# Optimization experiments

Hardware: AMD Instinct MI355X
Metric: run time of the kernel (lower is better)

Reference implementation:

```python
import jax, jax.numpy as jnp
import numpy as np

EPS = 1e-5
NH_MHA = 8
NH_GCN = 4


def _ln(x, w, b):
    m = x.mean(-1, keepdims=True)
    v = ((x - m) ** 2).mean(-1, keepdims=True)
    return (x - m) * jax.lax.rsqrt(v + EPS) * w + b


def _mha(t, in_w, in_b, out_w, out_b):
    # torch nn.MultiheadAttention (batch_first, eval mode -> no dropout)
    B, N, C = t.shape
    hd = C // NH_MHA
    qkv = t @ in_w.T + in_b
    q, k, v = jnp.split(qkv, 3, axis=-1)
    q = q.reshape(B, N, NH_MHA, hd)
    k = k.reshape(B, N, NH_MHA, hd)
    v = v.reshape(B, N, NH_MHA, hd)
    s = jnp.einsum('bihd,bjhd->bhij', q, k) * (1.0 / np.sqrt(hd))
    a = jax.nn.softmax(s, axis=-1)
    o = jnp.einsum('bhij,bjhd->bihd', a, v).reshape(B, N, C)
    return o @ out_w.T + out_b


def _gcn(x, v_w, v_b, e1_w, e1_b, eln_w, eln_b, e2_w, e2_b, o_w, o_b, n_w, n_b):
    # GraphConvolutionNetwork.forward (query/key branches are computed but
    # unused in the original -> omitted, identical math)
    B, N, C = x.shape
    hd = C // NH_GCN
    # edge MLP: split first linear so the [B,N,N,2C] concat is never built
    w1a, w1b = e1_w[:, :C], e1_w[:, C:]
    e = (x @ w1a.T)[:, :, None, :] + (x @ w1b.T)[:, None, :, :] + e1_b  # [B,N,N,C]
    e = jax.nn.gelu(_ln(e, eln_w, eln_b), approximate=False)
    ew = e @ e2_w.T + e2_b                 # [B,Ni,Nj,H]
    adj = jax.nn.softmax(ew, axis=2)       # softmax over Nj (== dim=-1 after permute in torch)
    v = (x @ v_w.T + v_b).reshape(B, N, NH_GCN, hd)
    out = jnp.einsum('bijh,bjhd->bihd', adj, v).reshape(B, N, C)
    out = out @ o_w.T + o_b
    return _ln(out + x, n_w, n_b)          # in_features == out_features -> residual


def reference(x, mha_in_w, mha_in_b, mha_out_w, mha_out_b,
              g0_v_w, g0_v_b, g0_e1_w, g0_e1_b, g0_eln_w, g0_eln_b, g0_e2_w, g0_e2_b, g0_o_w, g0_o_b, g0_n_w, g0_n_b,
              g1_v_w, g1_v_b, g1_e1_w, g1_e1_b, g1_eln_w, g1_eln_b, g1_e2_w, g1_e2_b, g1_o_w, g1_o_b, g1_n_w, g1_n_b,
              n1_w, n1_b, n2_w, n2_b,
              f1_w, f1_b, fln_w, fln_b, f2_w, f2_b):
    B, C, H, W = x.shape
    tokens = x.reshape(B, C, H * W).transpose(0, 2, 1)  # b c h w -> b (h w) c
    attn = _mha(tokens, mha_in_w, mha_in_b, mha_out_w, mha_out_b)
    attn = _ln(attn + tokens, n1_w, n1_b)
    g = _gcn(attn, g0_v_w, g0_v_b, g0_e1_w, g0_e1_b, g0_eln_w, g0_eln_b, g0_e2_w, g0_e2_b, g0_o_w, g0_o_b, g0_n_w, g0_n_b)
    g = _gcn(g, g1_v_w, g1_v_b, g1_e1_w, g1_e1_b, g1_eln_w, g1_eln_b, g1_e2_w, g1_e2_b, g1_o_w, g1_o_b, g1_n_w, g1_n_b)
    g = _ln(g, n2_w, n2_b)
    cat = jnp.concatenate([attn, g], axis=-1)           # [B,N,2C]
    f = cat @ f1_w.T + f1_b
    f = jax.nn.gelu(_ln(f, fln_w, fln_b), approximate=False)
    f = f @ f2_w.T + f2_b
    out = tokens + f
    return out.transpose(0, 2, 1).reshape(B, C, H, W)


def setup_inputs() -> dict:
    key = jax.random.key(0)
    ks = jax.random.split(key, 8)
    B, C, H, W = 2, 128, 24, 24
    f32 = jnp.float32

    def w(k, shape):
        return jax.random.normal(k, shape, f32) * 0.02

    d = {"x": jax.random.normal(ks[0], (B, C, H, W), f32)}
    d["mha_in_w"] = w(ks[1], (3 * C, C)); d["mha_in_b"] = jnp.zeros((3 * C,), f32)
    d["mha_out_w"] = w(ks[2], (C, C)); d["mha_out_b"] = jnp.zeros((C,), f32)
    for i in range(2):
        kk = jax.random.split(ks[3 + i], 4)
        p = f"g{i}_"
        d[p + "v_w"] = w(kk[0], (C, C)); d[p + "v_b"] = jnp.zeros((C,), f32)
        d[p + "e1_w"] = w(kk[1], (C, 2 * C)); d[p + "e1_b"] = jnp.zeros((C,), f32)
        d[p + "eln_w"] = jnp.ones((C,), f32); d[p + "eln_b"] = jnp.zeros((C,), f32)
        d[p + "e2_w"] = w(kk[2], (NH_GCN, C)); d[p + "e2_b"] = jnp.zeros((NH_GCN,), f32)
        d[p + "o_w"] = w(kk[3], (C, C)); d[p + "o_b"] = jnp.zeros((C,), f32)
        d[p + "n_w"] = jnp.ones((C,), f32); d[p + "n_b"] = jnp.zeros((C,), f32)
    d["n1_w"] = jnp.ones((C,), f32); d["n1_b"] = jnp.zeros((C,), f32)
    d["n2_w"] = jnp.ones((C,), f32); d["n2_b"] = jnp.zeros((C,), f32)
    d["f1_w"] = w(ks[5], (C, 2 * C)); d["f1_b"] = jnp.zeros((C,), f32)
    d["fln_w"] = jnp.ones((C,), f32); d["fln_b"] = jnp.zeros((C,), f32)
    d["f2_w"] = w(ks[6], (C, C)); d["f2_b"] = jnp.zeros((C,), f32)
    return d
```

## Files before the change

### kernel.cpp

```cpp
#include <hip/hip_runtime.h>
#include <hip/hip_fp16.h>
#include <math.h>

#define NN 576
#define EPSV 1e-5f

typedef _Float16 h2v __attribute__((ext_vector_type(2)));
__device__ __forceinline__ float fdot2f(__half2 a, __half2 b, float c) {
    return __builtin_amdgcn_fdot2(__builtin_bit_cast(h2v, a),
                                  __builtin_bit_cast(h2v, b), c, false);
}

__device__ __forceinline__ float gelu_exact(float x) {
    return 0.5f * x * (1.0f + erff(x * 0.70710678118654752f));
}

__global__ void k_tok(const float* __restrict__ x, float* __restrict__ tok) {
    int b = blockIdx.y;
    int idx = blockIdx.x * 256 + threadIdx.x;
    if (idx < NN * 128) {
        int n = idx >> 7, c = idx & 127;
        tok[(size_t)b * NN * 128 + idx] = x[((size_t)b * 128 + c) * NN + n];
    }
}

__global__ void k_prep(const float* __restrict__ mha_in_w,
                       const float* __restrict__ e1w0, const float* __restrict__ vw0,
                       const float* __restrict__ e1w1, const float* __restrict__ vw1,
                       const float* __restrict__ lnw0, const float* __restrict__ lnb0,
                       const float* __restrict__ e2w0,
                       const float* __restrict__ lnw1, const float* __restrict__ lnb1,
                       const float* __restrict__ e2w1,
                       float* __restrict__ wTq, float* __restrict__ wT0,
                       float* __restrict__ wT1, __half* __restrict__ wh) {
    int which = blockIdx.y;
    int idx = blockIdx.x * 256 + threadIdx.x;
    if (which == 3) {
        if (idx < 1536) {
            int l = idx / 768, i2 = idx - l * 768;
            const float* lw = l ? lnw1 : lnw0;
            const float* lb = l ? lnb1 : lnb0;
            const float* e2 = l ? e2w1 : e2w0;
            float v;
            if (i2 < 128)      v = lw[i2];
            else if (i2 < 256) v = lb[i2 - 128];
            else               v = e2[i2 - 256];
            wh[idx] = __float2half(v);
        }
        return;
    }
    int k = idx / 384, o = idx - k * 384;
    if (which == 0) {
        wTq[idx] = mha_in_w[o * 128 + k];
    } else {
        const float* e1w = (which == 1) ? e1w0 : e1w1;
        const float* vw  = (which == 1) ? vw0  : vw1;
        float v;
        if (o < 128)      v = e1w[o * 256 + k];
        else if (o < 256) v = e1w[(o - 128) * 256 + 128 + k];
        else              v = vw[(o - 256) * 128 + k];
        ((which == 1) ? wT0 : wT1)[idx] = v;
    }
}

template<bool CENTER>
__global__ __launch_bounds__(384) void k_gemmT(
    const float* __restrict__ A, const float* __restrict__ wT,
    const float* __restrict__ b0, const float* __restrict__ b1, const float* __restrict__ b2,
    float* __restrict__ out)
{
    const int t = threadIdx.x;
    const int r0 = blockIdx.x * 4;
    __shared__ float a_s[4][132];
    if (t < 128) {
        float4 v = *(const float4*)(A + (size_t)(r0 + (t >> 5)) * 128 + (t & 31) * 4);
        *(float4*)&a_s[t >> 5][(t & 31) * 4] = v;
    }
    __syncthreads();
    float acc[4] = {0.f, 0.f, 0.f, 0.f};
    #pragma unroll 8
    for (int k = 0; k < 128; ++k) {
        float w = wT[(size_t)k * 384 + t];
        acc[0] += a_s[0][k] * w;
        acc[1] += a_s[1][k] * w;
        acc[2] += a_s[2][k] * w;
        acc[3] += a_s[3][k] * w;
    }
    const float* bp = (t < 128) ? b0 : ((t < 256) ? b1 : b2);
    float bv = bp ? bp[t & 127] : 0.f;
    #pragma unroll
    for (int r = 0; r < 4; ++r) acc[r] += bv;

    if (CENTER) {
        __shared__ float redc[6][4];
        const int wv = t >> 6, ln = t & 63;
        #pragma unroll
        for (int r = 0; r < 4; ++r) {
            float xr = acc[r];
            #pragma unroll
            for (int off = 32; off > 0; off >>= 1) xr += __shfl_xor(xr, off);
            if (ln == 0) redc[wv][r] = xr;
        }
        __syncthreads();
        if (t < 256) {
            const int ch = t >> 7;
            #pragma unroll
            for (int r = 0; r < 4; ++r) {
                float mean = (redc[2 * ch][r] + redc[2 * ch + 1][r]) * (1.0f / 128.0f);
                acc[r] -= mean;
            }
        }
    }
    if (t < 256) {
        #pragma unroll
        for (int r = 0; r < 4; ++r)
            ((__half*)(out + (size_t)(r0 + r) * 384))[t] = __float2half(acc[r]);
    } else {
        #pragma unroll
        for (int r = 0; r < 4; ++r)
            out[(size_t)(r0 + r) * 384 + t] = acc[r];
    }
}

__global__ __launch_bounds__(256) void k_score(
    const float* __restrict__ qkv, __half* __restrict__ sc)
{
    const int jt = blockIdx.x, it = blockIdx.y, b = blockIdx.z;
    const int i0 = it * 16, j0 = jt * 16;
    const int t = threadIdx.x;
    __shared__ __half q_s[16][136], k_s[16][136];
    for (int idx = t; idx < 512; idx += 256) {
        int tile = idx >> 8, r = (idx >> 4) & 15, cq = idx & 15;
        const __half* src = (const __half*)(qkv + (size_t)(b * NN + (tile ? j0 : i0) + r) * 384)
                            + (tile ? 128 : 0) + cq * 8;
        __half* dst = tile ? &k_s[r][cq * 8] : &q_s[r][cq * 8];
        *(uint4*)dst = *(const uint4*)src;
    }
    __syncthreads();
    const int ti = t >> 4, tj = t & 15;
    const uint4* qr = (const uint4*)q_s[ti];
    const uint4* kr = (const uint4*)k_s[tj];
    float acc[8] = {0.f,0.f,0.f,0.f,0.f,0.f,0.f,0.f};
    #pragma unroll
    for (int sstep = 0; sstep < 16; ++sstep) {
        uint4 q4 = qr[sstep], k4 = kr[sstep];
        const __half2* qh = (const __half2*)&q4;
        const __half2* kh = (const __half2*)&k4;
        #pragma unroll
        for (int p = 0; p < 4; ++p)
            acc[sstep >> 1] = fdot2f(qh[p], kh[p], acc[sstep >> 1]);
    }
    __half2 h[4];
    #pragma unroll
    for (int p = 0; p < 4; ++p)
        h[p] = __floats2half2_rn(acc[2 * p] * 0.25f, acc[2 * p + 1] * 0.25f);
    *(uint4*)(sc + ((size_t)(b * NN + i0 + ti) * NN + j0 + tj) * 8) = *(uint4*)h;
}

__global__ __launch_bounds__(256) void k_edge(
    const float* __restrict__ qkv, const __half* __restrict__ wh,
    const float* __restrict__ e2b, __half* __restrict__ ew)
{
    const int jt = blockIdx.x, it = blockIdx.y, b = blockIdx.z;
    const int i0 = it * 16, j0 = jt * 16;
    const int t = threadIdx.x;
    __shared__ __half ua_s[16][136], wb_s[16][136], wh_s[768];

    for (int idx = t; idx < 512; idx += 256) {
        int tile = idx >> 8, r = (idx >> 4) & 15, cq = idx & 15;
        const __half* src = (const __half*)(qkv + (size_t)(b * NN + (tile ? j0 : i0) + r) * 384)
                            + (tile ? 128 : 0) + cq * 8;
        __half* dst = tile ? &wb_s[r][cq * 8] : &ua_s[r][cq * 8];
        *(uint4*)dst = *(const uint4*)src;
    }
    if (t < 96) *(uint4*)&wh_s[t * 8] = *(const uint4*)&wh[t * 8];
    __syncthreads();

    const int ti = t >> 4, tj = t & 15;
    const uint4* uar = (const uint4*)ua_s[ti];
    const uint4* wbr = (const uint4*)wb_s[tj];

    float s2 = 0.f;
    #pragma unroll
    for (int sstep = 0; sstep < 16; ++sstep) {
        uint4 u4 = uar[sstep], w4 = wbr[sstep];
        const __half2* uh = (const __half2*)&u4;
        const __half2* whp = (const __half2*)&w4;
        #pragma unroll
        for (int p = 0; p < 4; ++p) {
            __half2 e = __hadd2(uh[p], whp[p]);
            s2 = fdot2f(e, e, s2);
        }
    }
    const float rstd = rsqrtf(s2 * (1.0f / 128.0f) + EPSV);
    const __half2 rh   = __float2half2_rn(rstd);
    const __half2 cexp = __float2half2_rn(-2.4554672f);
    const __half2 one2 = __float2half2_rn(1.0f);

    float p0 = 0.f, p1 = 0.f, p2 = 0.f, p3 = 0.f;
    #pragma unroll 4
    for (int sstep = 0; sstep < 16; ++sstep) {
        uint4 u4 = uar[sstep], w4 = wbr[sstep];
        uint4 lw4 = *(const uint4*)&wh_s[sstep * 8];
        uint4 lb4 = *(const uint4*)&wh_s[128 + sstep * 8];
        uint4 q04 = *(const uint4*)&wh_s[256 + sstep * 8];
        uint4 q14 = *(const uint4*)&wh_s[384 + sstep * 8];
        uint4 q24 = *(const uint4*)&wh_s[512 + sstep * 8];
        uint4 q34 = *(const uint4*)&wh_s[640 + sstep * 8];
        const __half2* uh  = (const __half2*)&u4;
        const __half2* whp = (const __half2*)&w4;
        const __half2* lwh = (const __half2*)&lw4;
        const __half2* lbh = (const __half2*)&lb4;
        const __half2* q0h = (const __half2*)&q04;
        const __half2* q1h = (const __half2*)&q14;
        const __half2* q2h = (const __half2*)&q24;
        const __half2* q3h = (const __half2*)&q34;
        #pragma unroll
        for (int p = 0; p < 4; ++p) {
            __half2 e   = __hadd2(uh[p], whp[p]);
            __half2 rlw = __hmul2(rh, lwh[p]);
            __half2 nrm = __hfma2(e, rlw, lbh[p]);
            __half2 z   = __hmul2(nrm, cexp);
            __half2 ex  = h2exp2(z);
            __half2 den = __hadd2(ex, one2);
            __half2 rr  = h2rcp(den);
            __half2 g   = __hmul2(nrm, rr);
            p0 = fdot2f(g, q0h[p], p0);
            p1 = fdot2f(g, q1h[p], p1);
            p2 = fdot2f(g, q2h[p], p2);
            p3 = fdot2f(g, q3h[p], p3);
        }
    }
    __half2 h01 = __floats2half2_rn(p0 + e2b[0], p1 + e2b[1]);
    __half2 h23 = __floats2half2_rn(p2 + e2b[2], p3 + e2b[3]);
    __half* dst = ew + ((size_t)(b * NN + i0 + ti) * NN + j0 + tj) * 4;
    *(__half2*)dst = h01;
    *(__half2*)(dst + 2) = h23;
}

template<int NH>
__global__ __launch_bounds__(256) void k_agg(
    const float* __restrict__ resid, const float* __restrict__ vbuf,
    const __half* __restrict__ sc,
    const float* __restrict__ ow, const float* __restrict__ ob,
    const float* __restrict__ nw, const float* __restrict__ nb,
    float* __restrict__ outp)
{
    constexpr int GL = 256 / NH;
    constexpr int NE = NN / GL;
    const int bi = blockIdx.x;
    const int b = bi / NN, i = bi - b * NN;
    const int t = threadIdx.x;

    __shared__ float st_m[NH], st_i[NH];
    __shared__ float aggp[8][128];
    __shared__ float agg_s[128];
    __shared__ float op[2][128];
    __shared__ float red1[4], red2[4];

    const __half* srow = sc + (size_t)(b * NN + i) * NN * NH;

    {
        const int h = t / GL, jl = t % GL;
        float sv[NE];
        #pragma unroll
        for (int k = 0; k < NE; ++k)
            sv[k] = __half2float(srow[(size_t)(jl + k * GL) * NH + h]);
        float mx = -1e30f;
        #pragma unroll
        for (int k = 0; k < NE; ++k) mx = fmaxf(mx, sv[k]);
        #pragma unroll
        for (int off = GL / 2; off > 0; off >>= 1) mx = fmaxf(mx, __shfl_xor(mx, off));
        float sm = 0.f;
        #pragma unroll
        for (int k = 0; k < NE; ++k) sm += __expf(sv[k] - mx);
        #pragma unroll
        for (int off = GL / 2; off > 0; off >>= 1) sm += __shfl_xor(sm, off);
        if (jl == 0) { st_m[h] = mx; st_i[h] = 1.0f / sm; }
    }
    __syncthreads();

    {
        const int c4 = (t & 31) * 4, jg = t >> 5;
        const int h2 = c4 >> ((NH == 8) ? 4 : 5);
        const float m2 = st_m[h2], inv2 = st_i[h2];
        float4 acc = {0.f, 0.f, 0.f, 0.f};
        const float* vb = vbuf + 256 + c4;
        #pragma unroll 4
        for (int j = jg; j < NN; j += 8) {
            float p = __expf(__half2float(srow[(size_t)j * NH + h2]) - m2);
            const float4 v4 = *(const float4*)(vb + (size_t)(b * NN + j) * 384);
            acc.x += p * v4.x; acc.y += p * v4.y; acc.z += p * v4.z; acc.w += p * v4.w;
        }
        acc.x *= inv2; acc.y *= inv2; acc.z *= inv2; acc.w *= inv2;
        *(float4*)&aggp[jg][c4] = acc;
    }
    __syncthreads();
    if (t < 128) {
        float s = 0.f;
        #pragma unroll
        for (int gq = 0; gq < 8; ++gq) s += aggp[gq][t];
        agg_s[t] = s;
    }
    __syncthreads();

    {
        const int c = t & 127, half = t >> 7;
        float o = 0.f;
        const float4* wr = (const float4*)(ow + (size_t)c * 128 + half * 64);
        const float4* ar = (const float4*)(agg_s + half * 64);
        #pragma unroll
        for (int kq = 0; kq < 16; ++kq) {
            float4 w = wr[kq], a = ar[kq];
            o += w.x * a.x + w.y * a.y + w.z * a.z + w.w * a.w;
        }
        op[half][c] = o;
    }
    __syncthreads();
    float val = 0.f;
    if (t < 128)
        val = op[0][t] + op[1][t] + ob[t] + resid[(size_t)(b * NN + i) * 128 + t];

    float s1 = val, s2 = val * val;
    #pragma unroll
    for (int off = 32; off > 0; off >>= 1) {
        s1 += __shfl_xor(s1, off);
        s2 += __shfl_xor(s2, off);
    }
    if ((t & 63) == 0) { red1[t >> 6] = s1; red2[t >> 6] = s2; }
    __syncthreads();
    float tot1 = red1[0] + red1[1] + red1[2] + red1[3];
    float tot2 = red2[0] + red2[1] + red2[2] + red2[3];
    float mean = tot1 * (1.0f / 128.0f);
    float var = tot2 * (1.0f / 128.0f) - mean * mean;
    float rstd = rsqrtf(var + EPSV);
    if (t < 128)
        outp[(size_t)(b * NN + i) * 128 + t] = (val - mean) * rstd * nw[t] + nb[t];
}

__global__ __launch_bounds__(128) void k_final(
    const float* __restrict__ tok, const float* __restrict__ attn, const float* __restrict__ g,
    const float* __restrict__ n2w, const float* __restrict__ n2b,
    const float* __restrict__ f1w, const float* __restrict__ f1b,
    const float* __restrict__ flnw, const float* __restrict__ flnb,
    const float* __restrict__ f2w, const float* __restrict__ f2b,
    float* __restrict__ out)
{
    const int bi = blockIdx.x;
    const int b = bi / NN, i = bi - b * NN;
    const int t = threadIdx.x;
    __shared__ float cat_s[256];
    __shared__ float gl_s[128];
    __shared__ float red1[2], red2[2];

    const size_t row = (size_t)(b * NN + i) * 128;
    cat_s[t] = attn[row + t];
    float gv = g[row + t];
    {
        float s1 = gv, s2 = gv * gv;
        #pragma unroll
        for (int off = 32; off > 0; off >>= 1) { s1 += __shfl_xor(s1, off); s2 += __shfl_xor(s2, off); }
        if ((t & 63) == 0) { red1[t >> 6] = s1; red2[t >> 6] = s2; }
        __syncthreads();
        float mean = (red1[0] + red1[1]) * (1.0f / 128.0f);
        float var = (red2[0] + red2[1]) * (1.0f / 128.0f) - mean * mean;
        float rstd = rsqrtf(var + EPSV);
        cat_s[128 + t] = (gv - mean) * rstd * n2w[t] + n2b[t];
    }
    __syncthreads();
    float f = f1b[t];
    {
        const float4* wr = reinterpret_cast<const float4*>(f1w + (size_t)t * 256);
        const float4* cr = reinterpret_cast<const float4*>(cat_s);
        #pragma unroll 8
        for (int kq = 0; kq < 64; ++kq) {
            float4 w = wr[kq], c = cr[kq];
            f += w.x * c.x + w.y * c.y + w.z * c.z + w.w * c.w;
        }
    }
    {
        float s1 = f, s2 = f * f;
        #pragma unroll
        for (int off = 32; off > 0; off >>= 1) { s1 += __shfl_xor(s1, off); s2 += __shfl_xor(s2, off); }
        __syncthreads();
        if ((t & 63) == 0) { red1[t >> 6] = s1; red2[t >> 6] = s2; }
        __syncthreads();
        float mean = (red1[0] + red1[1]) * (1.0f / 128.0f);
        float var = (red2[0] + red2[1]) * (1.0f / 128.0f) - mean * mean;
        float rstd = rsqrtf(var + EPSV);
        float nrm = (f - mean) * rstd * flnw[t] + flnb[t];
        gl_s[t] = gelu_exact(nrm);
    }
    __syncthreads();
    float o = f2b[t];
    {
        const float4* wr = reinterpret_cast<const float4*>(f2w + (size_t)t * 128);
        const float4* gr = reinterpret_cast<const float4*>(gl_s);
        #pragma unroll 8
        for (int kq = 0; kq < 32; ++kq) {
            float4 w = wr[kq], gg = gr[kq];
            o += w.x * gg.x + w.y * gg.y + w.z * gg.z + w.w * gg.w;
        }
    }
    out[((size_t)b * 128 + t) * NN + i] = tok[row + t] + o;
}

extern "C" void kernel_launch(void* const* d_in, const int* in_sizes, int n_in,
                              void* d_out, int out_size, void* d_ws, size_t ws_size,
                              hipStream_t stream) {
    const float* x         = (const float*)d_in[0];
    const float* mha_in_b  = (const float*)d_in[2];
    const float* mha_out_w = (const float*)d_in[3];
    const float* mha_out_b = (const float*)d_in[4];
    const float* gv_w[2]  = {(const float*)d_in[5],  (const float*)d_in[17]};
    const float* gv_b[2]  = {(const float*)d_in[6],  (const float*)d_in[18]};
    const float* ge1_w[2] = {(const float*)d_in[7],  (const float*)d_in[19]};
    const float* ge1_b[2] = {(const float*)d_in[8],  (const float*)d_in[20]};
    const float* geln_w[2]= {(const float*)d_in[9],  (const float*)d_in[21]};
    const float* geln_b[2]= {(const float*)d_in[10], (const float*)d_in[22]};
    const float* ge2_w[2] = {(const float*)d_in[11], (const float*)d_in[23]};
    const float* ge2_b[2] = {(const float*)d_in[12], (const float*)d_in[24]};
    const float* go_w[2]  = {(const float*)d_in[13], (const float*)d_in[25]};
    const float* go_b[2]  = {(const float*)d_in[14], (const float*)d_in[26]};
    const float* gn_w[2]  = {(const float*)d_in[15], (const float*)d_in[27]};
    const float* gn_b[2]  = {(const float*)d_in[16], (const float*)d_in[28]};
    const float* n1w = (const float*)d_in[29];
    const float* n1b = (const float*)d_in[30];
    const float* n2w = (const float*)d_in[31];
    const float* n2b = (const float*)d_in[32];
    const float* f1w = (const float*)d_in[33];
    const float* f1b = (const float*)d_in[34];
    const float* flnw = (const float*)d_in[35];
    const float* flnb = (const float*)d_in[36];
    const float* f2w = (const float*)d_in[37];
    const float* f2b = (const float*)d_in[38];

    float* ws     = (float*)d_ws;
    float* tokens = ws;
    float* attn   = tokens + 147456;
    float* g      = attn + 147456;
    float* qkv    = g + 147456;
    float* wTq    = qkv + 442368;
    float* wT0    = wTq + 49152;
    float* wT1    = wT0 + 49152;
    __half* wh    = (__half*)(wT1 + 49152);
    __half* sc    = wh + 2048;
    __half* ewh   = sc;

    k_tok<<<dim3(288, 2), 256, 0, stream>>>(x, tokens);
    k_prep<<<dim3(192, 4), 256, 0, stream>>>((const float*)d_in[1],
        ge1_w[0], gv_w[0], ge1_w[1], gv_w[1],
        geln_w[0], geln_b[0], ge2_w[0],
        geln_w[1], geln_b[1], ge2_w[1],
        wTq, wT0, wT1, wh);

    k_gemmT<false><<<288, 384, 0, stream>>>(tokens, wTq,
        mha_in_b, mha_in_b + 128, mha_in_b + 256, qkv);
    k_score<<<dim3(36, 36, 2), 256, 0, stream>>>(qkv, sc);
    k_agg<8><<<1152, 256, 0, stream>>>(tokens, qkv, sc, mha_out_w, mha_out_b,
                                       n1w, n1b, attn);

    for (int l = 0; l < 2; ++l) {
        const float* xin = (l == 0) ? attn : g;
        const float* wTl = (l == 0) ? wT0 : wT1;
        k_gemmT<true><<<288, 384, 0, stream>>>(xin, wTl,
            nullptr, ge1_b[l], gv_b[l], qkv);
        k_edge<<<dim3(36, 36, 2), 256, 0, stream>>>(qkv, wh + l * 768,
                                                    ge2_b[l], ewh);
        k_agg<4><<<1152, 256, 0, stream>>>(xin, qkv, ewh, go_w[l], go_b[l],
                                           gn_w[l], gn_b[l], g);
    }
    k_final<<<1152, 128, 0, stream>>>(tokens, attn, g, n2w, n2b,
        f1w, f1b, flnw, flnb, f2w, f2b, (float*)d_out);
}
```

Baseline: 229.2 us.

## Fuse setup kernels, fold final FFN into last aggregation, cache softmax probs in LDS

Merges the token transpose and weight prep into one setup launch, and fuses the final norm/FFN stage into the last GCN aggregation kernel so the final layer output never goes through global memory. The aggregation kernel now keeps exponentiated scores as fp16 in shared memory instead of re-reading scores and recomputing exp in the value pass. The edge kernel reorders the LayerNorm multiply. The changes cut launches and redundant exp/global reads, at the cost of more shared memory per block (lower occupancy) and fp16 rounding of the probabilities.

```diff
diff --git a/kernel.cpp b/kernel.cpp
--- a/kernel.cpp
+++ b/kernel.cpp
@@ -4,6 +4,7 @@
 
 #define NN 576
 #define EPSV 1e-5f
+#define PSTR 592
 
 typedef _Float16 h2v __attribute__((ext_vector_type(2)));
 __device__ __forceinline__ float fdot2f(__half2 a, __half2 b, float c) {
@@ -15,27 +16,26 @@
     return 0.5f * x * (1.0f + erff(x * 0.70710678118654752f));
 }
 
-__global__ void k_tok(const float* __restrict__ x, float* __restrict__ tok) {
-    int b = blockIdx.y;
-    int idx = blockIdx.x * 256 + threadIdx.x;
-    if (idx < NN * 128) {
-        int n = idx >> 7, c = idx & 127;
-        tok[(size_t)b * NN * 128 + idx] = x[((size_t)b * 128 + c) * NN + n];
-    }
-}
-
-__global__ void k_prep(const float* __restrict__ mha_in_w,
-                       const float* __restrict__ e1w0, const float* __restrict__ vw0,
-                       const float* __restrict__ e1w1, const float* __restrict__ vw1,
-                       const float* __restrict__ lnw0, const float* __restrict__ lnb0,
-                       const float* __restrict__ e2w0,
-                       const float* __restrict__ lnw1, const float* __restrict__ lnb1,
-                       const float* __restrict__ e2w1,
-                       float* __restrict__ wTq, float* __restrict__ wT0,
-                       float* __restrict__ wT1, __half* __restrict__ wh) {
-    int which = blockIdx.y;
-    int idx = blockIdx.x * 256 + threadIdx.x;
-    if (which == 3) {
+__global__ void k_setup(const float* __restrict__ x, float* __restrict__ tok,
+                        const float* __restrict__ mha_in_w,
+                        const float* __restrict__ e1w0, const float* __restrict__ vw0,
+                        const float* __restrict__ e1w1, const float* __restrict__ vw1,
+                        const float* __restrict__ lnw0, const float* __restrict__ lnb0,
+                        const float* __restrict__ e2w0,
+                        const float* __restrict__ lnw1, const float* __restrict__ lnb1,
+                        const float* __restrict__ e2w1,
+                        float* __restrict__ wTq, float* __restrict__ wT0,
+                        float* __restrict__ wT1, __half* __restrict__ wh) {
+    const int which = blockIdx.y;
+    const int idx = blockIdx.x * 256 + threadIdx.x;
+    if (which < 2) {
+        if (idx < NN * 128) {
+            int n = idx >> 7, c = idx & 127;
+            tok[(size_t)which * NN * 128 + idx] = x[((size_t)which * 128 + c) * NN + n];
+        }
+        return;
+    }
+    if (which == 5) {
         if (idx < 1536) {
             int l = idx / 768, i2 = idx - l * 768;
             const float* lw = l ? lnw1 : lnw0;
@@ -49,17 +49,18 @@
         }
         return;
     }
+    if (idx >= 49152) return;
     int k = idx / 384, o = idx - k * 384;
-    if (which == 0) {
+    if (which == 2) {
         wTq[idx] = mha_in_w[o * 128 + k];
     } else {
-        const float* e1w = (which == 1) ? e1w0 : e1w1;
-        const float* vw  = (which == 1) ? vw0  : vw1;
+        const float* e1w = (which == 3) ? e1w0 : e1w1;
+        const float* vw  = (which == 3) ? vw0  : vw1;
         float v;
         if (o < 128)      v = e1w[o * 256 + k];
         else if (o < 256) v = e1w[(o - 128) * 256 + 128 + k];
         else              v = vw[(o - 256) * 128 + k];
-        ((which == 1) ? wT0 : wT1)[idx] = v;
+        ((which == 3) ? wT0 : wT1)[idx] = v;
     }
 }
 
@@ -218,8 +219,8 @@
         #pragma unroll
         for (int p = 0; p < 4; ++p) {
             __half2 e   = __hadd2(uh[p], whp[p]);
-            __half2 rlw = __hmul2(rh, lwh[p]);
-            __half2 nrm = __hfma2(e, rlw, lbh[p]);
+            __half2 t1  = __hmul2(e, lwh[p]);
+            __half2 nrm = __hfma2(t1, rh, lbh[p]);
             __half2 z   = __hmul2(nrm, cexp);
             __half2 ex  = h2exp2(z);
             __half2 den = __hadd2(ex, one2);
@@ -238,13 +239,19 @@
     *(__half2*)(dst + 2) = h23;
 }
 
-template<int NH>
+template<int NH, bool FINAL>
 __global__ __launch_bounds__(256) void k_agg(
     const float* __restrict__ resid, const float* __restrict__ vbuf,
     const __half* __restrict__ sc,
     const float* __restrict__ ow, const float* __restrict__ ob,
     const float* __restrict__ nw, const float* __restrict__ nb,
-    float* __restrict__ outp)
+    float* __restrict__ outp,
+    const float* __restrict__ tok, const float* __restrict__ attn,
+    const float* __restrict__ n2w, const float* __restrict__ n2b,
+    const float* __restrict__ f1w, const float* __restrict__ f1b,
+    const float* __restrict__ flnw, const float* __restrict__ flnb,
+    const float* __restrict__ f2w, const float* __restrict__ f2b,
+    float* __restrict__ finout)
 {
     constexpr int GL = 256 / NH;
     constexpr int NE = NN / GL;
@@ -252,11 +259,14 @@
     const int b = bi / NN, i = bi - b * NN;
     const int t = threadIdx.x;
 
-    __shared__ float st_m[NH], st_i[NH];
+    __shared__ __half p_lds[NH * PSTR];
+    __shared__ float st_i[NH];
     __shared__ float aggp[8][128];
     __shared__ float agg_s[128];
     __shared__ float op[2][128];
     __shared__ float red1[4], red2[4];
+    __shared__ float cat_s[256], gl_s[128];
+    __shared__ float red3[4], red4[4], red5[2], red6[2];
 
     const __half* srow = sc + (size_t)(b * NN + i) * NN * NH;
 
@@ -273,22 +283,27 @@
         for (int off = GL / 2; off > 0; off >>= 1) mx = fmaxf(mx, __shfl_xor(mx, off));
         float sm = 0.f;
         #pragma unroll
-        for (int k = 0; k < NE; ++k) sm += __expf(sv[k] - mx);
+        for (int k = 0; k < NE; ++k) {
+            float e = __expf(sv[k] - mx);
+            sm += e;
+            p_lds[h * PSTR + jl + k * GL] = __float2half(e);
+        }
         #pragma unroll
         for (int off = GL / 2; off > 0; off >>= 1) sm += __shfl_xor(sm, off);
-        if (jl == 0) { st_m[h] = mx; st_i[h] = 1.0f / sm; }
+        if (jl == 0) st_i[h] = 1.0f / sm;
     }
     __syncthreads();
 
     {
         const int c4 = (t & 31) * 4, jg = t >> 5;
         const int h2 = c4 >> ((NH == 8) ? 4 : 5);
-        const float m2 = st_m[h2], inv2 = st_i[h2];
+        const float inv2 = st_i[h2];
         float4 acc = {0.f, 0.f, 0.f, 0.f};
         const float* vb = vbuf + 256 + c4;
+        const __half* ph = p_lds + h2 * PSTR;
         #pragma unroll 4
         for (int j = jg; j < NN; j += 8) {
-            float p = __expf(__half2float(srow[(size_t)j * NH + h2]) - m2);
+            float p = __half2float(ph[j]);
             const float4 v4 = *(const float4*)(vb + (size_t)(b * NN + j) * 384);
             acc.x += p * v4.x; acc.y += p * v4.y; acc.z += p * v4.z; acc.w += p * v4.w;
         }
@@ -317,9 +332,10 @@
         op[half][c] = o;
     }
     __syncthreads();
+    const size_t row = (size_t)(b * NN + i) * 128;
     float val = 0.f;
     if (t < 128)
-        val = op[0][t] + op[1][t] + ob[t] + resid[(size_t)(b * NN + i) * 128 + t];
+        val = op[0][t] + op[1][t] + ob[t] + resid[row + t];
 
     float s1 = val, s2 = val * val;
     #pragma unroll
@@ -334,75 +350,79 @@
     float mean = tot1 * (1.0f / 128.0f);
     float var = tot2 * (1.0f / 128.0f) - mean * mean;
     float rstd = rsqrtf(var + EPSV);
-    if (t < 128)
-        outp[(size_t)(b * NN + i) * 128 + t] = (val - mean) * rstd * nw[t] + nb[t];
-}
-
-__global__ __launch_bounds__(128) void k_final(
-    const float* __restrict__ tok, const float* __restrict__ attn, const float* __restrict__ g,
-    const float* __restrict__ n2w, const float* __restrict__ n2b,
-    const float* __restrict__ f1w, const float* __restrict__ f1b,
-    const float* __restrict__ flnw, const float* __restrict__ flnb,
-    const float* __restrict__ f2w, const float* __restrict__ f2b,
-    float* __restrict__ out)
-{
-    const int bi = blockIdx.x;
-    const int b = bi / NN, i = bi - b * NN;
-    const int t = threadIdx.x;
-    __shared__ float cat_s[256];
-    __shared__ float gl_s[128];
-    __shared__ float red1[2], red2[2];
-
-    const size_t row = (size_t)(b * NN + i) * 128;
-    cat_s[t] = attn[row + t];
-    float gv = g[row + t];
-    {
-        float s1 = gv, s2 = gv * gv;
-        #pragma unroll
-        for (int off = 32; off > 0; off >>= 1) { s1 += __shfl_xor(s1, off); s2 += __shfl_xor(s2, off); }
-        if ((t & 63) == 0) { red1[t >> 6] = s1; red2[t >> 6] = s2; }
-        __syncthreads();
-        float mean = (red1[0] + red1[1]) * (1.0f / 128.0f);
-        float var = (red2[0] + red2[1]) * (1.0f / 128.0f) - mean * mean;
-        float rstd = rsqrtf(var + EPSV);
-        cat_s[128 + t] = (gv - mean) * rstd * n2w[t] + n2b[t];
-    }
-    __syncthreads();
-    float f = f1b[t];
-    {
-        const float4* wr = reinterpret_cast<const float4*>(f1w + (size_t)t * 256);
-        const float4* cr = reinterpret_cast<const float4*>(cat_s);
-        #pragma unroll 8
-        for (int kq = 0; kq < 64; ++kq) {
+    float gval = 0.f;
+    if (t < 128) gval = (val - mean) * rstd * nw[t] + nb[t];
+
+    if (!FINAL) {
+        if (t < 128) outp[row + t] = gval;
+        return;
+    }
+
+    {
+        float a1 = gval, a2 = gval * gval;
+        #pragma unroll
+        for (int off = 32; off > 0; off >>= 1) { a1 += __shfl_xor(a1, off); a2 += __shfl_xor(a2, off); }
+        if ((t & 63) == 0) { red3[t >> 6] = a1; red4[t >> 6] = a2; }
+    }
+    __syncthreads();
+    {
+        float m2 = (red3[0] + red3[1] + red3[2] + red3[3]) * (1.0f / 128.0f);
+        float v2 = (red4[0] + red4[1] + red4[2] + red4[3]) * (1.0f / 128.0f) - m2 * m2;
+        float r2 = rsqrtf(v2 + EPSV);
+        if (t < 128) {
+            cat_s[t] = attn[row + t];
+            cat_s[128 + t] = (gval - m2) * r2 * n2w[t] + n2b[t];
+        }
+    }
+    __syncthreads();
+    {
+        const int o = t & 127, half = t >> 7;
+        float f = 0.f;
+        const float4* wr = (const float4*)(f1w + (size_t)o * 256 + half * 128);
+        const float4* cr = (const float4*)(cat_s + half * 128);
+        #pragma unroll
+        for (int kq = 0; kq < 32; ++kq) {
             float4 w = wr[kq], c = cr[kq];
             f += w.x * c.x + w.y * c.y + w.z * c.z + w.w * c.w;
         }
-    }
-    {
-        float s1 = f, s2 = f * f;
-        #pragma unroll
-        for (int off = 32; off > 0; off >>= 1) { s1 += __shfl_xor(s1, off); s2 += __shfl_xor(s2, off); }
-        __syncthreads();
-        if ((t & 63) == 0) { red1[t >> 6] = s1; red2[t >> 6] = s2; }
-        __syncthreads();
-        float mean = (red1[0] + red1[1]) * (1.0f / 128.0f);
-        float var = (red2[0] + red2[1]) * (1.0f / 128.0f) - mean * mean;
-        float rstd = rsqrtf(var + EPSV);
-        float nrm = (f - mean) * rstd * flnw[t] + flnb[t];
-        gl_s[t] = gelu_exact(nrm);
-    }
-    __syncthreads();
-    float o = f2b[t];
-    {
-        const float4* wr = reinterpret_cast<const float4*>(f2w + (size_t)t * 128);
-        const float4* gr = reinterpret_cast<const float4*>(gl_s);
-        #pragma unroll 8
-        for (int kq = 0; kq < 32; ++kq) {
+        op[half][o] = f;
+    }
+    __syncthreads();
+    float fv = 0.f;
+    if (t < 128) fv = op[0][t] + op[1][t] + f1b[t];
+    {
+        float a1 = fv, a2 = fv * fv;
+        #pragma unroll
+        for (int off = 32; off > 0; off >>= 1) { a1 += __shfl_xor(a1, off); a2 += __shfl_xor(a2, off); }
+        if (t < 128 && (t & 63) == 0) { red5[t >> 6] = a1; red6[t >> 6] = a2; }
+    }
+    __syncthreads();
+    {
+        float m3 = (red5[0] + red5[1]) * (1.0f / 128.0f);
+        float v3 = (red6[0] + red6[1]) * (1.0f / 128.0f) - m3 * m3;
+        float r3 = rsqrtf(v3 + EPSV);
+        if (t < 128) {
+            float nrm = (fv - m3) * r3 * flnw[t] + flnb[t];
+            gl_s[t] = gelu_exact(nrm);
+        }
+    }
+    __syncthreads();
+    {
+        const int o = t & 127, half = t >> 7;
+        float f = 0.f;
+        const float4* wr = (const float4*)(f2w + (size_t)o * 128 + half * 64);
+        const float4* gr = (const float4*)(gl_s + half * 64);
+        #pragma unroll
+        for (int kq = 0; kq < 16; ++kq) {
             float4 w = wr[kq], gg = gr[kq];
-            o += w.x * gg.x + w.y * gg.y + w.z * gg.z + w.w * gg.w;
-        }
-    }
-    out[((size_t)b * 128 + t) * NN + i] = tok[row + t] + o;
+            f += w.x * gg.x + w.y * gg.y + w.z * gg.z + w.w * gg.w;
+        }
+        op[half][o] = f;
+    }
+    __syncthreads();
+    if (t < 128)
+        finout[((size_t)b * 128 + t) * NN + i] =
+            tok[row + t] + op[0][t] + op[1][t] + f2b[t];
 }
 
 extern "C" void kernel_launch(void* const* d_in, const int* in_sizes, int n_in,
@@ -447,8 +467,7 @@
     __half* sc    = wh + 2048;
     __half* ewh   = sc;
 
-    k_tok<<<dim3(288, 2), 256, 0, stream>>>(x, tokens);
-    k_prep<<<dim3(192, 4), 256, 0, stream>>>((const float*)d_in[1],
+    k_setup<<<dim3(288, 6), 256, 0, stream>>>(x, tokens, (const float*)d_in[1],
         ge1_w[0], gv_w[0], ge1_w[1], gv_w[1],
         geln_w[0], geln_b[0], ge2_w[0],
         geln_w[1], geln_b[1], ge2_w[1],
@@ -457,8 +476,10 @@
     k_gemmT<false><<<288, 384, 0, stream>>>(tokens, wTq,
         mha_in_b, mha_in_b + 128, mha_in_b + 256, qkv);
     k_score<<<dim3(36, 36, 2), 256, 0, stream>>>(qkv, sc);
-    k_agg<8><<<1152, 256, 0, stream>>>(tokens, qkv, sc, mha_out_w, mha_out_b,
-                                       n1w, n1b, attn);
+    k_agg<8, false><<<1152, 256, 0, stream>>>(tokens, qkv, sc, mha_out_w, mha_out_b,
+        n1w, n1b, attn,
+        nullptr, nullptr, nullptr, nullptr, nullptr, nullptr, nullptr, nullptr,
+        nullptr, nullptr, nullptr);
 
     for (int l = 0; l < 2; ++l) {
         const float* xin = (l == 0) ? attn : g;
@@ -467,9 +488,16 @@
             nullptr, ge1_b[l], gv_b[l], qkv);
         k_edge<<<dim3(36, 36, 2), 256, 0, stream>>>(qkv, wh + l * 768,
                                                     ge2_b[l], ewh);
-        k_agg<4><<<1152, 256, 0, stream>>>(xin, qkv, ewh, go_w[l], go_b[l],
-                                           gn_w[l], gn_b[l], g);
-    }
-    k_final<<<1152, 128, 0, stream>>>(tokens, attn, g, n2w, n2b,
-        f1w, f1b, flnw, flnb, f2w, f2b, (float*)d_out);
-}
+        if (l == 0) {
+            k_agg<4, false><<<1152, 256, 0, stream>>>(xin, qkv, ewh, go_w[l], go_b[l],
+                gn_w[l], gn_b[l], g,
+                nullptr, nullptr, nullptr, nullptr, nullptr, nullptr, nullptr, nullptr,
+                nullptr, nullptr, nullptr);
+        } else {
+            k_agg<4, true><<<1152, 256, 0, stream>>>(xin, qkv, ewh, go_w[l], go_b[l],
+                gn_w[l], gn_b[l], nullptr,
+                tokens, attn, n2w, n2b, f1w, f1b, flnw, flnb, f2w, f2b,
+                (float*)d_out);
+        }
+    }
+}
```

Measured after the change: 220.4 us. -3.8%, faster.
